# Kernel tuning notes

Measured on AMD Instinct MI355X. Metric: run time of the kernel, lower is better.

Reference implementation:

```python
import jax, jax.numpy as jnp
import numpy as np

K = 4  # topk neighbors (default of match())
ALPHA = 0.0  # blend factor (default of match())


def setup_inputs() -> dict:
    key = jax.random.key(0)
    k1, k2 = jax.random.split(key)
    B, D, T, N = 32, 32, 16384, 128
    source = jax.random.normal(k1, (B, D, T), dtype=jnp.float32)
    tokens = jax.random.normal(k2, (1, D, N), dtype=jnp.float32)  # nn.Parameter
    return {"source": source, "tokens": tokens}


def reference(source, tokens):
    # source: (B, D, T); tokens: (1, D, N)
    ref = tokens[0].T                                   # (N, D) unnormalized reference
    s = jnp.swapaxes(source, 1, 2)                      # (B, T, D)
    s_n = s / jnp.linalg.norm(s, axis=2, keepdims=True)
    r_n = ref / jnp.linalg.norm(ref, axis=1, keepdims=True)
    cos_sims = jnp.einsum('btd,nd->btn', s_n, r_n)      # (B, T, N)
    _, idx = jax.lax.top_k(cos_sims, K)                 # (B, T, K)
    gathered = ref[idx]                                 # (B, T, K, D) gather of unnormalized refs
    result = gathered.mean(axis=2)                      # (B, T, D)
    out = jnp.swapaxes(result, 1, 2)                    # (B, D, T)
    return out * (1.0 - ALPHA) + source * ALPHA
```

## Files before the change

### kernel.cpp

```cpp
#include <hip/hip_runtime.h>
#include <math.h>

constexpr int B = 32, D = 32, T = 16384, N = 128;

__device__ __forceinline__ float np_pairwise32_sq(const float* v) {
#pragma clang fp contract(off)
    float r[8];
    #pragma unroll
    for (int j = 0; j < 8; ++j) r[j] = v[j] * v[j];
    #pragma unroll
    for (int i = 8; i < 32; i += 8) {
        #pragma unroll
        for (int j = 0; j < 8; ++j) r[j] += v[i + j] * v[i + j];
    }
    return ((r[0] + r[1]) + (r[2] + r[3])) + ((r[4] + r[5]) + (r[6] + r[7]));
}

__global__ __launch_bounds__(256) void ve_kernel(
    const float* __restrict__ source,
    const float* __restrict__ tokens,
    float* __restrict__ out)
{
#pragma clang fp contract(off)
    __shared__ float rn[N][D];
    __shared__ float rf[N][D + 1];

    for (int i = threadIdx.x; i < N * D; i += 256) {
        int d = i >> 7, n = i & (N - 1);
        rf[n][d] = tokens[i];
    }
    __syncthreads();

    if (threadIdx.x < N) {
        int n = threadIdx.x;
        float tq[D];
        #pragma unroll
        for (int d = 0; d < D; ++d) tq[d] = rf[n][d];
        float nrm = sqrtf(np_pairwise32_sq(tq));
        #pragma unroll
        for (int d = 0; d < D; ++d) rn[n][d] = tq[d] / nrm;
    }
    __syncthreads();

    int gid = blockIdx.x * 256 + threadIdx.x;
    int b = gid >> 14, t = gid & (T - 1);

    const float* src = source + (size_t)b * D * T + t;
    float s[D];
    #pragma unroll
    for (int d = 0; d < D; ++d) s[d] = src[(size_t)d * T];

    float nrm = sqrtf(np_pairwise32_sq(s));
    float sn[D];
    #pragma unroll
    for (int d = 0; d < D; ++d) sn[d] = s[d] / nrm;

    float tv0 = -INFINITY, tv1 = -INFINITY, tv2 = -INFINITY, tv3 = -INFINITY;
    int ti0 = 0, ti1 = 0, ti2 = 0, ti3 = 0;

    for (int n = 0; n < N; ++n) {
        const float4* rw = reinterpret_cast<const float4*>(&rn[n][0]);
        float acc = 0.0f;
        #pragma unroll
        for (int k = 0; k < 8; ++k) {
            float4 q = rw[k];
            acc += sn[4 * k + 0] * q.x;
            acc += sn[4 * k + 1] * q.y;
            acc += sn[4 * k + 2] * q.z;
            acc += sn[4 * k + 3] * q.w;
        }

        bool c0 = acc > tv0, c1 = acc > tv1, c2 = acc > tv2, c3 = acc > tv3;
        float nv3 = c3 ? (c2 ? tv2 : acc) : tv3;  int ni3 = c3 ? (c2 ? ti2 : n) : ti3;
        float nv2 = c2 ? (c1 ? tv1 : acc) : tv2;  int ni2 = c2 ? (c1 ? ti1 : n) : ti2;
        float nv1 = c1 ? (c0 ? tv0 : acc) : tv1;  int ni1 = c1 ? (c0 ? ti0 : n) : ti1;
        float nv0 = c0 ? acc : tv0;               int ni0 = c0 ? n : ti0;
        tv0 = nv0; tv1 = nv1; tv2 = nv2; tv3 = nv3;
        ti0 = ni0; ti1 = ni1; ti2 = ni2; ti3 = ni3;
    }

    float* dst = out + (size_t)b * D * T + t;
    #pragma unroll
    for (int d = 0; d < D; ++d) {
        float sum = ((rf[ti0][d] + rf[ti1][d]) + rf[ti2][d]) + rf[ti3][d];
        dst[(size_t)d * T] = sum * 0.25f;
    }
}

extern "C" void kernel_launch(void* const* d_in, const int* in_sizes, int n_in,
                              void* d_out, int out_size, void* d_ws, size_t ws_size,
                              hipStream_t stream) {
    const float* source = (const float*)d_in[0];
    const float* tokens = (const float*)d_in[1];
    float* out = (float*)d_out;

    dim3 grid((B * T) / 256), block(256);
    ve_kernel<<<grid, block, 0, stream>>>(source, tokens, out);
}
```

Measured before the change: 139.3 us.

## Process two tokens per thread with FMA dot products and margin-checked exact fallback

Each thread now handles two time positions, t and t+T/2, so every shared-memory load of a normalized reference row is reused for two dot products. The dot products use FMAs split into even and odd accumulators, which shortens the dependency chain but can round differently from the sequential reference. To keep top-k selection exact, the kernel tracks the fifth-best score, and when the gap between 4th and 5th is within a small margin it recomputes that token with the original sequential non-FMA dot product. The grid is halved, and each thread holds more registers, which may lower occupancy.

```diff
diff --git a/kernel.cpp b/kernel.cpp
--- a/kernel.cpp
+++ b/kernel.cpp
@@ -2,6 +2,8 @@
 #include <math.h>
 
 constexpr int B = 32, D = 32, T = 16384, N = 128;
+constexpr int HALF_T = T / 2;
+constexpr float MARG = 2.5e-5f;
 
 __device__ __forceinline__ float np_pairwise32_sq(const float* v) {
 #pragma clang fp contract(off)
@@ -16,12 +18,46 @@
     return ((r[0] + r[1]) + (r[2] + r[3])) + ((r[4] + r[5]) + (r[6] + r[7]));
 }
 
+__device__ __forceinline__ float np_seq_dot(const float* __restrict__ sn,
+                                            const float4* __restrict__ rw) {
+#pragma clang fp contract(off)
+    float acc = 0.0f;
+    #pragma unroll
+    for (int k = 0; k < 8; ++k) {
+        float4 q = rw[k];
+        acc += sn[4 * k + 0] * q.x;
+        acc += sn[4 * k + 1] * q.y;
+        acc += sn[4 * k + 2] * q.z;
+        acc += sn[4 * k + 3] * q.w;
+    }
+    return acc;
+}
+
+#define INSERT_TRACK(v, n, tv0, tv1, tv2, tv3, ti0, ti1, ti2, ti3, m5)      \
+    {                                                                       \
+        float old3 = tv3;                                                   \
+        bool c0 = (v) > tv0, c1 = (v) > tv1, c2 = (v) > tv2, c3 = (v) > tv3;\
+        tv3 = c3 ? (c2 ? tv2 : (v)) : tv3;  ti3 = c3 ? (c2 ? ti2 : (n)) : ti3; \
+        tv2 = c2 ? (c1 ? tv1 : (v)) : tv2;  ti2 = c2 ? (c1 ? ti1 : (n)) : ti2; \
+        tv1 = c1 ? (c0 ? tv0 : (v)) : tv1;  ti1 = c1 ? (c0 ? ti0 : (n)) : ti1; \
+        tv0 = c0 ? (v) : tv0;               ti0 = c0 ? (n) : ti0;           \
+        m5 = fmaxf(m5, fminf((v), old3));                                   \
+    }
+
+#define INSERT4(v, n, tv0, tv1, tv2, tv3, ti0, ti1, ti2, ti3)               \
+    {                                                                       \
+        bool c0 = (v) > tv0, c1 = (v) > tv1, c2 = (v) > tv2, c3 = (v) > tv3;\
+        tv3 = c3 ? (c2 ? tv2 : (v)) : tv3;  ti3 = c3 ? (c2 ? ti2 : (n)) : ti3; \
+        tv2 = c2 ? (c1 ? tv1 : (v)) : tv2;  ti2 = c2 ? (c1 ? ti1 : (n)) : ti2; \
+        tv1 = c1 ? (c0 ? tv0 : (v)) : tv1;  ti1 = c1 ? (c0 ? ti0 : (n)) : ti1; \
+        tv0 = c0 ? (v) : tv0;               ti0 = c0 ? (n) : ti0;           \
+    }
+
 __global__ __launch_bounds__(256) void ve_kernel(
     const float* __restrict__ source,
     const float* __restrict__ tokens,
     float* __restrict__ out)
 {
-#pragma clang fp contract(off)
     __shared__ float rn[N][D];
     __shared__ float rf[N][D + 1];
 
@@ -43,47 +79,76 @@
     __syncthreads();
 
     int gid = blockIdx.x * 256 + threadIdx.x;
-    int b = gid >> 14, t = gid & (T - 1);
+    int b = gid >> 13;
+    int t = gid & (HALF_T - 1);
 
-    const float* src = source + (size_t)b * D * T + t;
-    float s[D];
-    #pragma unroll
-    for (int d = 0; d < D; ++d) s[d] = src[(size_t)d * T];
+    const float* src0 = source + (size_t)b * D * T + t;
 
-    float nrm = sqrtf(np_pairwise32_sq(s));
-    float sn[D];
-    #pragma unroll
-    for (int d = 0; d < D; ++d) sn[d] = s[d] / nrm;
+    float sn0[D], sn1[D];
+    {
+        float s0[D], s1[D];
+        #pragma unroll
+        for (int d = 0; d < D; ++d) {
+            s0[d] = src0[(size_t)d * T];
+            s1[d] = src0[(size_t)d * T + HALF_T];
+        }
+        float n0 = sqrtf(np_pairwise32_sq(s0));
+        float n1 = sqrtf(np_pairwise32_sq(s1));
+        #pragma unroll
+        for (int d = 0; d < D; ++d) { sn0[d] = s0[d] / n0; sn1[d] = s1[d] / n1; }
+    }
 
-    float tv0 = -INFINITY, tv1 = -INFINITY, tv2 = -INFINITY, tv3 = -INFINITY;
-    int ti0 = 0, ti1 = 0, ti2 = 0, ti3 = 0;
+    float av0 = -INFINITY, av1 = -INFINITY, av2 = -INFINITY, av3 = -INFINITY;
+    int   ai0 = 0, ai1 = 0, ai2 = 0, ai3 = 0;
+    float bv0 = -INFINITY, bv1 = -INFINITY, bv2 = -INFINITY, bv3 = -INFINITY;
+    int   bi0 = 0, bi1 = 0, bi2 = 0, bi3 = 0;
+    float m5a = -INFINITY, m5b = -INFINITY;
 
     for (int n = 0; n < N; ++n) {
         const float4* rw = reinterpret_cast<const float4*>(&rn[n][0]);
-        float acc = 0.0f;
+        float a_e = 0.f, a_o = 0.f, b_e = 0.f, b_o = 0.f;
         #pragma unroll
         for (int k = 0; k < 8; ++k) {
             float4 q = rw[k];
-            acc += sn[4 * k + 0] * q.x;
-            acc += sn[4 * k + 1] * q.y;
-            acc += sn[4 * k + 2] * q.z;
-            acc += sn[4 * k + 3] * q.w;
+            a_e = __builtin_fmaf(sn0[4 * k + 0], q.x, a_e);
+            a_o = __builtin_fmaf(sn0[4 * k + 1], q.y, a_o);
+            a_e = __builtin_fmaf(sn0[4 * k + 2], q.z, a_e);
+            a_o = __builtin_fmaf(sn0[4 * k + 3], q.w, a_o);
+            b_e = __builtin_fmaf(sn1[4 * k + 0], q.x, b_e);
+            b_o = __builtin_fmaf(sn1[4 * k + 1], q.y, b_o);
+            b_e = __builtin_fmaf(sn1[4 * k + 2], q.z, b_e);
+            b_o = __builtin_fmaf(sn1[4 * k + 3], q.w, b_o);
         }
+        float va = a_e + a_o;
+        float vb = b_e + b_o;
+        INSERT_TRACK(va, n, av0, av1, av2, av3, ai0, ai1, ai2, ai3, m5a);
+        INSERT_TRACK(vb, n, bv0, bv1, bv2, bv3, bi0, bi1, bi2, bi3, m5b);
+    }
 
-        bool c0 = acc > tv0, c1 = acc > tv1, c2 = acc > tv2, c3 = acc > tv3;
-        float nv3 = c3 ? (c2 ? tv2 : acc) : tv3;  int ni3 = c3 ? (c2 ? ti2 : n) : ti3;
-        float nv2 = c2 ? (c1 ? tv1 : acc) : tv2;  int ni2 = c2 ? (c1 ? ti1 : n) : ti2;
-        float nv1 = c1 ? (c0 ? tv0 : acc) : tv1;  int ni1 = c1 ? (c0 ? ti0 : n) : ti1;
-        float nv0 = c0 ? acc : tv0;               int ni0 = c0 ? n : ti0;
-        tv0 = nv0; tv1 = nv1; tv2 = nv2; tv3 = nv3;
-        ti0 = ni0; ti1 = ni1; ti2 = ni2; ti3 = ni3;
+    if (av3 - m5a <= MARG) {
+        av0 = av1 = av2 = av3 = -INFINITY;
+        ai0 = ai1 = ai2 = ai3 = 0;
+        for (int n = 0; n < N; ++n) {
+            float v = np_seq_dot(sn0, reinterpret_cast<const float4*>(&rn[n][0]));
+            INSERT4(v, n, av0, av1, av2, av3, ai0, ai1, ai2, ai3);
+        }
+    }
+    if (bv3 - m5b <= MARG) {
+        bv0 = bv1 = bv2 = bv3 = -INFINITY;
+        bi0 = bi1 = bi2 = bi3 = 0;
+        for (int n = 0; n < N; ++n) {
+            float v = np_seq_dot(sn1, reinterpret_cast<const float4*>(&rn[n][0]));
+            INSERT4(v, n, bv0, bv1, bv2, bv3, bi0, bi1, bi2, bi3);
+        }
     }
 
     float* dst = out + (size_t)b * D * T + t;
     #pragma unroll
     for (int d = 0; d < D; ++d) {
-        float sum = ((rf[ti0][d] + rf[ti1][d]) + rf[ti2][d]) + rf[ti3][d];
-        dst[(size_t)d * T] = sum * 0.25f;
+        float sa = ((rf[ai0][d] + rf[ai1][d]) + rf[ai2][d]) + rf[ai3][d];
+        float sb = ((rf[bi0][d] + rf[bi1][d]) + rf[bi2][d]) + rf[bi3][d];
+        dst[(size_t)d * T] = sa * 0.25f;
+        dst[(size_t)d * T + HALF_T] = sb * 0.25f;
     }
 }
 
@@ -94,6 +159,6 @@
     const float* tokens = (const float*)d_in[1];
     float* out = (float*)d_out;
 
-    dim3 grid((B * T) / 256), block(256);
+    dim3 grid((B * T / 2) / 256), block(256);
     ve_kernel<<<grid, block, 0, stream>>>(source, tokens, out);
 }
```

Measured after the change: 190.7 us. 1.37x slower.

## Use fast unnormalized FMA dot products with exact-recompute fallback for near-ties

Applied to the files above, without the earlier changes.

The main top-4 scan now computes dot products with the raw source vector using two FMA accumulators, skipping the per-element normalization divide and the strict sequential, contraction-free summation. It also tracks the fifth-best score, and when the gap between fourth and fifth falls within a margin scaled by the norm, it recomputes the whole scan with the original bit-exact normalized sequential arithmetic. The aim is to shorten the dependency chain and cut instruction count in the hot loop while keeping the same index selection as the reference. The cost is extra tracking work and a divergent slow path for threads with near-ties, and correctness depends on the margin being large enough to cover rounding differences.

```diff
diff --git a/kernel.cpp b/kernel.cpp
--- a/kernel.cpp
+++ b/kernel.cpp
@@ -2,6 +2,7 @@
 #include <math.h>
 
 constexpr int B = 32, D = 32, T = 16384, N = 128;
+constexpr float MARG = 2e-5f;
 
 __device__ __forceinline__ float np_pairwise32_sq(const float* v) {
 #pragma clang fp contract(off)
@@ -16,12 +17,42 @@
     return ((r[0] + r[1]) + (r[2] + r[3])) + ((r[4] + r[5]) + (r[6] + r[7]));
 }
 
+__device__ __forceinline__ float np_seq_dot(const float* __restrict__ sn,
+                                            const float4* __restrict__ rw) {
+#pragma clang fp contract(off)
+    float acc = 0.0f;
+    #pragma unroll
+    for (int k = 0; k < 8; ++k) {
+        float4 q = rw[k];
+        acc += sn[4 * k + 0] * q.x;
+        acc += sn[4 * k + 1] * q.y;
+        acc += sn[4 * k + 2] * q.z;
+        acc += sn[4 * k + 3] * q.w;
+    }
+    return acc;
+}
+
+#define INSERT4(v, n)                                                        \
+    {                                                                        \
+        bool c0 = (v) > tv0, c1 = (v) > tv1, c2 = (v) > tv2, c3 = (v) > tv3; \
+        tv3 = c3 ? (c2 ? tv2 : (v)) : tv3;  ti3 = c3 ? (c2 ? ti2 : (n)) : ti3; \
+        tv2 = c2 ? (c1 ? tv1 : (v)) : tv2;  ti2 = c2 ? (c1 ? ti1 : (n)) : ti2; \
+        tv1 = c1 ? (c0 ? tv0 : (v)) : tv1;  ti1 = c1 ? (c0 ? ti0 : (n)) : ti1; \
+        tv0 = c0 ? (v) : tv0;               ti0 = c0 ? (n) : ti0;            \
+    }
+
+#define INSERT_TRACK(v, n)                                                   \
+    {                                                                        \
+        float old3 = tv3;                                                    \
+        INSERT4(v, n);                                                       \
+        m5 = fmaxf(m5, fminf((v), old3));                                    \
+    }
+
 __global__ __launch_bounds__(256) void ve_kernel(
     const float* __restrict__ source,
     const float* __restrict__ tokens,
     float* __restrict__ out)
 {
-#pragma clang fp contract(off)
     __shared__ float rn[N][D];
     __shared__ float rf[N][D + 1];
 
@@ -51,32 +82,36 @@
     for (int d = 0; d < D; ++d) s[d] = src[(size_t)d * T];
 
     float nrm = sqrtf(np_pairwise32_sq(s));
-    float sn[D];
-    #pragma unroll
-    for (int d = 0; d < D; ++d) sn[d] = s[d] / nrm;
 
     float tv0 = -INFINITY, tv1 = -INFINITY, tv2 = -INFINITY, tv3 = -INFINITY;
-    int ti0 = 0, ti1 = 0, ti2 = 0, ti3 = 0;
+    int   ti0 = 0, ti1 = 0, ti2 = 0, ti3 = 0;
+    float m5 = -INFINITY;
 
     for (int n = 0; n < N; ++n) {
         const float4* rw = reinterpret_cast<const float4*>(&rn[n][0]);
-        float acc = 0.0f;
+        float a_e = 0.f, a_o = 0.f;
         #pragma unroll
         for (int k = 0; k < 8; ++k) {
             float4 q = rw[k];
-            acc += sn[4 * k + 0] * q.x;
-            acc += sn[4 * k + 1] * q.y;
-            acc += sn[4 * k + 2] * q.z;
-            acc += sn[4 * k + 3] * q.w;
+            a_e = __builtin_fmaf(s[4 * k + 0], q.x, a_e);
+            a_o = __builtin_fmaf(s[4 * k + 1], q.y, a_o);
+            a_e = __builtin_fmaf(s[4 * k + 2], q.z, a_e);
+            a_o = __builtin_fmaf(s[4 * k + 3], q.w, a_o);
         }
+        float v = a_e + a_o;
+        INSERT_TRACK(v, n);
+    }
 
-        bool c0 = acc > tv0, c1 = acc > tv1, c2 = acc > tv2, c3 = acc > tv3;
-        float nv3 = c3 ? (c2 ? tv2 : acc) : tv3;  int ni3 = c3 ? (c2 ? ti2 : n) : ti3;
-        float nv2 = c2 ? (c1 ? tv1 : acc) : tv2;  int ni2 = c2 ? (c1 ? ti1 : n) : ti2;
-        float nv1 = c1 ? (c0 ? tv0 : acc) : tv1;  int ni1 = c1 ? (c0 ? ti0 : n) : ti1;
-        float nv0 = c0 ? acc : tv0;               int ni0 = c0 ? n : ti0;
-        tv0 = nv0; tv1 = nv1; tv2 = nv2; tv3 = nv3;
-        ti0 = ni0; ti1 = ni1; ti2 = ni2; ti3 = ni3;
+    if (tv3 - m5 <= MARG * nrm) {
+        float sn[D];
+        #pragma unroll
+        for (int d = 0; d < D; ++d) sn[d] = s[d] / nrm;
+        tv0 = tv1 = tv2 = tv3 = -INFINITY;
+        ti0 = ti1 = ti2 = ti3 = 0;
+        for (int n = 0; n < N; ++n) {
+            float v = np_seq_dot(sn, reinterpret_cast<const float4*>(&rn[n][0]));
+            INSERT4(v, n);
+        }
     }
 
     float* dst = out + (size_t)b * D * T + t;
```

New measurement: 158.2 us. +13.6%, slower.

## Use unnormalized packed-FMA dot products with margin-checked exact fallback for top-k

Applied to the files above, without the earlier changes.

Token normalization moves to a separate one-block kernel that writes to workspace, so the main kernel no longer repeats it per block. The main scan skips dividing the source by its norm, computes dots with packed 2-wide FMAs read from global memory, and updates the top-4 using med3/max instructions. It tracks the 5th-best value, and when the 4th/5th gap is within a margin scaled by the norm, it reruns the exact sequential-order normalized dot for that thread, so tie ordering still matches the reference. The risk is divergence on the fallback path and reading reference rows from global/L1 instead of LDS.

```diff
diff --git a/kernel.cpp b/kernel.cpp
--- a/kernel.cpp
+++ b/kernel.cpp
@@ -1,7 +1,10 @@
 #include <hip/hip_runtime.h>
 #include <math.h>
 
+typedef float f32x2 __attribute__((ext_vector_type(2)));
+
 constexpr int B = 32, D = 32, T = 16384, N = 128;
+constexpr float MARG = 2e-5f;
 
 __device__ __forceinline__ float np_pairwise32_sq(const float* v) {
 #pragma clang fp contract(off)
@@ -16,13 +19,75 @@
     return ((r[0] + r[1]) + (r[2] + r[3])) + ((r[4] + r[5]) + (r[6] + r[7]));
 }
 
+__device__ __forceinline__ float np_pairwise32_sq2(const f32x2* v) {
+#pragma clang fp contract(off)
+    float r[8];
+    #pragma unroll
+    for (int j = 0; j < 8; ++j) {
+        float x = (j & 1) ? v[j >> 1].y : v[j >> 1].x;
+        r[j] = x * x;
+    }
+    #pragma unroll
+    for (int i = 8; i < 32; i += 8) {
+        #pragma unroll
+        for (int j = 0; j < 8; ++j) {
+            int e = i + j;
+            float x = (e & 1) ? v[e >> 1].y : v[e >> 1].x;
+            r[j] += x * x;
+        }
+    }
+    return ((r[0] + r[1]) + (r[2] + r[3])) + ((r[4] + r[5]) + (r[6] + r[7]));
+}
+
+__device__ __forceinline__ float np_seq_dot_g(const float* __restrict__ sn,
+                                              const float4* __restrict__ rw) {
+#pragma clang fp contract(off)
+    float acc = 0.0f;
+    #pragma unroll
+    for (int k = 0; k < 8; ++k) {
+        float4 q = rw[k];
+        acc += sn[4 * k + 0] * q.x;
+        acc += sn[4 * k + 1] * q.y;
+        acc += sn[4 * k + 2] * q.z;
+        acc += sn[4 * k + 3] * q.w;
+    }
+    return acc;
+}
+
+__global__ void norm_tokens_kernel(const float* __restrict__ tokens,
+                                   float* __restrict__ rn_g) {
+    int n = threadIdx.x;
+    if (n < N) {
+        float tq[D];
+        #pragma unroll
+        for (int d = 0; d < D; ++d) tq[d] = tokens[d * N + n];
+        float nrm = sqrtf(np_pairwise32_sq(tq));
+        #pragma unroll
+        for (int d = 0; d < D; ++d) rn_g[n * D + d] = tq[d] / nrm;
+    }
+}
+
+#define INSERT_STEP(v, n)                                                    \
+    {                                                                        \
+        bool c0 = (v) > t0, c1 = (v) > t1, c2 = (v) > t2, c3 = (v) > t3;     \
+        float nt0 = fmaxf(t0, (v));                                          \
+        float nt1 = __builtin_amdgcn_fmed3f((v), t1, t0);                    \
+        float nt2 = __builtin_amdgcn_fmed3f((v), t2, t1);                    \
+        float nt3 = __builtin_amdgcn_fmed3f((v), t3, t2);                    \
+        int ni0 = c0 ? (n) : i0;                                             \
+        int ni1 = c1 ? (c0 ? i0 : (n)) : i1;                                 \
+        int ni2 = c2 ? (c1 ? i1 : (n)) : i2;                                 \
+        int ni3 = c3 ? (c2 ? i2 : (n)) : i3;                                 \
+        t0 = nt0; t1 = nt1; t2 = nt2; t3 = nt3;                              \
+        i0 = ni0; i1 = ni1; i2 = ni2; i3 = ni3;                              \
+    }
+
 __global__ __launch_bounds__(256) void ve_kernel(
     const float* __restrict__ source,
+    const float* __restrict__ rn_g,
     const float* __restrict__ tokens,
     float* __restrict__ out)
 {
-#pragma clang fp contract(off)
-    __shared__ float rn[N][D];
     __shared__ float rf[N][D + 1];
 
     for (int i = threadIdx.x; i < N * D; i += 256) {
@@ -31,58 +96,58 @@
     }
     __syncthreads();
 
-    if (threadIdx.x < N) {
-        int n = threadIdx.x;
-        float tq[D];
-        #pragma unroll
-        for (int d = 0; d < D; ++d) tq[d] = rf[n][d];
-        float nrm = sqrtf(np_pairwise32_sq(tq));
-        #pragma unroll
-        for (int d = 0; d < D; ++d) rn[n][d] = tq[d] / nrm;
-    }
-    __syncthreads();
-
     int gid = blockIdx.x * 256 + threadIdx.x;
     int b = gid >> 14, t = gid & (T - 1);
 
     const float* src = source + (size_t)b * D * T + t;
-    float s[D];
+    f32x2 s2[16];
     #pragma unroll
-    for (int d = 0; d < D; ++d) s[d] = src[(size_t)d * T];
+    for (int k = 0; k < 16; ++k) {
+        s2[k].x = src[(size_t)(2 * k) * T];
+        s2[k].y = src[(size_t)(2 * k + 1) * T];
+    }
+    float nrm = sqrtf(np_pairwise32_sq2(s2));
 
-    float nrm = sqrtf(np_pairwise32_sq(s));
-    float sn[D];
-    #pragma unroll
-    for (int d = 0; d < D; ++d) sn[d] = s[d] / nrm;
+    float t0 = -INFINITY, t1 = -INFINITY, t2 = -INFINITY, t3 = -INFINITY;
+    float m5 = -INFINITY;
+    int i0 = 0, i1 = 0, i2 = 0, i3 = 0;
 
-    float tv0 = -INFINITY, tv1 = -INFINITY, tv2 = -INFINITY, tv3 = -INFINITY;
-    int ti0 = 0, ti1 = 0, ti2 = 0, ti3 = 0;
+    const f32x2* rn2 = (const f32x2*)rn_g;
+    #pragma unroll 2
+    for (int n = 0; n < N; ++n) {
+        const f32x2* r2 = rn2 + (n << 4);
+        f32x2 e = {0.f, 0.f}, o = {0.f, 0.f};
+        #pragma unroll
+        for (int k = 0; k < 16; k += 2) {
+            e += s2[k] * r2[k];
+            o += s2[k + 1] * r2[k + 1];
+        }
+        f32x2 h = e + o;
+        float v = h.x + h.y;
 
-    for (int n = 0; n < N; ++n) {
-        const float4* rw = reinterpret_cast<const float4*>(&rn[n][0]);
-        float acc = 0.0f;
+        m5 = fmaxf(m5, fminf(v, t3));
+        INSERT_STEP(v, n);
+    }
+
+    if (t3 - m5 <= MARG * nrm) {
+        float sn[32];
         #pragma unroll
-        for (int k = 0; k < 8; ++k) {
-            float4 q = rw[k];
-            acc += sn[4 * k + 0] * q.x;
-            acc += sn[4 * k + 1] * q.y;
-            acc += sn[4 * k + 2] * q.z;
-            acc += sn[4 * k + 3] * q.w;
+        for (int k = 0; k < 16; ++k) {
+            sn[2 * k]     = s2[k].x / nrm;
+            sn[2 * k + 1] = s2[k].y / nrm;
         }
-
-        bool c0 = acc > tv0, c1 = acc > tv1, c2 = acc > tv2, c3 = acc > tv3;
-        float nv3 = c3 ? (c2 ? tv2 : acc) : tv3;  int ni3 = c3 ? (c2 ? ti2 : n) : ti3;
-        float nv2 = c2 ? (c1 ? tv1 : acc) : tv2;  int ni2 = c2 ? (c1 ? ti1 : n) : ti2;
-        float nv1 = c1 ? (c0 ? tv0 : acc) : tv1;  int ni1 = c1 ? (c0 ? ti0 : n) : ti1;
-        float nv0 = c0 ? acc : tv0;               int ni0 = c0 ? n : ti0;
-        tv0 = nv0; tv1 = nv1; tv2 = nv2; tv3 = nv3;
-        ti0 = ni0; ti1 = ni1; ti2 = ni2; ti3 = ni3;
+        t0 = t1 = t2 = t3 = -INFINITY;
+        i0 = i1 = i2 = i3 = 0;
+        for (int n = 0; n < N; ++n) {
+            float v = np_seq_dot_g(sn, (const float4*)rn_g + (n << 3));
+            INSERT_STEP(v, n);
+        }
     }
 
     float* dst = out + (size_t)b * D * T + t;
     #pragma unroll
     for (int d = 0; d < D; ++d) {
-        float sum = ((rf[ti0][d] + rf[ti1][d]) + rf[ti2][d]) + rf[ti3][d];
+        float sum = ((rf[i0][d] + rf[i1][d]) + rf[i2][d]) + rf[i3][d];
         dst[(size_t)d * T] = sum * 0.25f;
     }
 }
@@ -93,7 +158,8 @@
     const float* source = (const float*)d_in[0];
     const float* tokens = (const float*)d_in[1];
     float* out = (float*)d_out;
+    float* rn_g = (float*)d_ws;
 
-    dim3 grid((B * T) / 256), block(256);
-    ve_kernel<<<grid, block, 0, stream>>>(source, tokens, out);
+    norm_tokens_kernel<<<1, 128, 0, stream>>>(tokens, rn_g);
+    ve_kernel<<<(B * T) / 256, 256, 0, stream>>>(source, rn_g, tokens, out);
 }
```

New measurement: 155.6 us. 11.6% more time.
